# Optimization experiments

Measured on AMD Instinct MI355X. Metric: run time of the kernel, lower is better.

The kernel has to match this reference:

```python
import jax, jax.numpy as jnp
import numpy as np

B, M, N, T = 16, 16, 32, 80


def setup_inputs() -> dict:
    key = jax.random.key(0)
    ks = jax.random.split(key, 20)
    p = lambda k, shp: jax.random.normal(k, shp, jnp.float32) * 0.05
    return {
        "ego_traj": jax.random.normal(ks[0], (B, M, T, 6), jnp.float32),
        "ego_encoding": jax.random.normal(ks[1], (B, 256), jnp.float32),
        "agents_traj": jax.random.normal(ks[2], (B, M, N, T, 3), jnp.float32),
        "agents_states": jax.random.normal(ks[3], (B, N, 11), jnp.float32),
        # interaction_feature_encoder: Linear(10,64) -> ReLU -> Linear(64,256)
        "enc_w1": p(ks[4], (10, 64)), "enc_b1": p(ks[5], (64,)),
        "enc_w2": p(ks[6], (64, 256)), "enc_b2": p(ks[7], (256,)),
        # interaction_feature_decoder: Linear(256,64) -> ELU -> Linear(64,4) -> Sigmoid
        "dec_w1": p(ks[8], (256, 64)), "dec_b1": p(ks[9], (64,)),
        "dec_w2": p(ks[10], (64, 4)), "dec_b2": p(ks[11], (4,)),
        # weights_decoder: Linear(256,64) -> ELU -> Linear(64,8) -> Softplus
        "wd_w1": p(ks[12], (256, 64)), "wd_b1": p(ks[13], (64,)),
        "wd_w2": p(ks[14], (64, 8)), "wd_b2": p(ks[15], (8,)),
        "timesteps": 80,
    }


def reference(ego_traj, ego_encoding, agents_traj, agents_states,
              enc_w1, enc_b1, enc_w2, enc_b2,
              dec_w1, dec_b1, dec_w2, dec_b2,
              wd_w1, wd_b1, wd_w2, wd_b2, timesteps):
    Tm = timesteps
    # ---- hardcoded ego features: B,M,4 ----
    speed = ego_traj[:, :, :Tm, 3]
    acc = ego_traj[:, :, :Tm, 4]
    jerk = jnp.diff(acc, axis=-1) / 0.1
    jerk = jnp.concatenate([jerk[:, :, :1], jerk], axis=-1)
    curvature = ego_traj[:, :, :Tm, 5]
    lat_acc = speed ** 2 * curvature
    hard = jnp.stack([
        -jnp.clip(speed.mean(-1), 0.0, 15.0) / 15.0,
        jnp.clip(jnp.abs(acc).mean(-1), 0.0, 4.0) / 4.0,
        jnp.clip(jnp.abs(jerk).mean(-1), 0.0, 6.0) / 6.0,
        jnp.clip(jnp.abs(lat_acc).mean(-1), 0.0, 5.0) / 5.0,
    ], axis=-1)  # B,M,4

    # ---- latent interaction features (vectorized over M) ----
    agent_mask = (agents_states.sum(-1) != 0).astype(ego_traj.dtype)  # B,N
    ry = agents_traj[:, :, :, :Tm, 2] - ego_traj[:, :, None, :Tm, 2]  # B,M,N,T
    ry = jnp.arctan2(jnp.sin(ry), jnp.cos(ry))
    rp = agents_traj[:, :, :, :Tm, :2] - ego_traj[:, :, None, :Tm, :2]
    rp = jnp.stack([rp[..., 0] * jnp.cos(ry), rp[..., 1] * jnp.sin(ry)], axis=-1)
    av = jnp.diff(agents_traj[:, :, :, :Tm, :2], axis=-2) / 0.1
    av = jnp.concatenate([av[:, :, :, :1, :], av], axis=-2)
    evx = ego_traj[:, :, :Tm, 3] * jnp.cos(ego_traj[:, :, :Tm, 2])  # B,M,T
    evy = ego_traj[:, :, :Tm, 3] * jnp.sin(ego_traj[:, :, :Tm, 2])
    rv = jnp.stack([(av[..., 0] - evx[:, :, None]) * jnp.cos(ry),
                    (av[..., 1] - evy[:, :, None]) * jnp.sin(ry)], axis=-1)
    rel = jnp.concatenate([rp, ry[..., None], rv], axis=-1)  # B,M,N,T,5
    aattr = jnp.broadcast_to(agents_states[:, None, :, None, 6:], rel.shape[:4] + (5,))
    attr = jnp.concatenate([rel, aattr], axis=-1) * agent_mask[:, None, :, None, None]  # B,M,N,T,10
    h = jax.nn.relu(attr @ enc_w1 + enc_b1) @ enc_w2 + enc_b2  # B,M,N,T,256
    feat = h.max(axis=2).mean(axis=2)  # max over agents, mean over time -> B,M,256
    inter = jax.nn.sigmoid(jax.nn.elu(feat @ dec_w1 + dec_b1) @ dec_w2 + dec_b2)  # B,M,4

    # ---- weights (variable_cost=False -> ones_like encoding) ----
    enc_in = jnp.ones_like(ego_encoding)
    weights = jax.nn.softplus(jax.nn.elu(enc_in @ wd_w1 + wd_b1) @ wd_w2 + wd_b2)  # B,8

    # ---- collision cost: B,M ----
    dist = jnp.linalg.norm(ego_traj[:, :, None, :Tm, :2] - agents_traj[:, :, :, :Tm, :2], axis=-1)
    coll = (jnp.exp(-0.2 * dist ** 2) * agent_mask[:, None, :, None]).sum((-1, -2))

    feats = jnp.concatenate([hard, inter], axis=-1)  # B,M,8
    scores = -jnp.sum(feats * weights[:, None, :], axis=-1) - 10.0 * coll
    ego_mask = ego_traj.sum(-1).sum(-1) != 0  # B,M
    scores = jnp.where(ego_mask, scores, -jnp.inf)
    return scores, weights
```

## Files before the change

### kernel.cpp

```cpp
#include <hip/hip_runtime.h>
#include <hip/hip_fp16.h>
#include <math.h>
#include <string.h>

typedef __attribute__((ext_vector_type(8))) short short8;
typedef __attribute__((ext_vector_type(8))) _Float16 f16x8;
typedef __attribute__((ext_vector_type(4))) _Float16 h4;
typedef __attribute__((ext_vector_type(2))) _Float16 h2;
typedef __attribute__((ext_vector_type(4))) float f32x4;

#define NB 16
#define NM 16
#define NN 32
#define NT 80
#define TC 16
#define NP 5
#define CH 4
#define NCH 8

#define WS_WTS 0
#define WS_BF 16
#define WS_BB 8208
#define WS_BASE 24592
#define WS_BM_STRIDE 1344
#define WS_SC_OFF 1280

__device__ __forceinline__ short f2h(float f) {
  _Float16 h = (_Float16)f;
  short s; memcpy(&s, &h, 2); return s;
}
__device__ __forceinline__ unsigned h2bits(h2 h) {
  unsigned u; memcpy(&u, &h, 4); return u;
}
__device__ __forceinline__ h2 bits2h(unsigned u) {
  h2 h; memcpy(&h, &u, 4); return h;
}

__global__ void prep_kernel(const float* __restrict__ agents_states,
                            const float* __restrict__ enc_w1,
                            const float* __restrict__ enc_b1,
                            const float* __restrict__ enc_w2,
                            const float* __restrict__ wd_w1,
                            const float* __restrict__ wd_b1,
                            const float* __restrict__ wd_w2,
                            const float* __restrict__ wd_b2,
                            float* __restrict__ ws,
                            float* __restrict__ out) {
  const int blk = blockIdx.x;
  const int tid = threadIdx.x;
  if (blk < NB) {
    __shared__ float smask[NN];
    if (tid < NN) {
      const float* st = agents_states + ((size_t)blk * NN + tid) * 11;
      float s = 0.f;
      for (int i = 0; i < 11; ++i) s += st[i];
      smask[tid] = (s != 0.f) ? 1.f : 0.f;
    }
    __syncthreads();
    h2* bb = reinterpret_cast<h2*>(ws + WS_BB) + blk * (NN * 32);
    for (int e = tid; e < NN * 32; e += 256) {
      int n = e >> 5, jp = e & 31;
      const float* st = agents_states + ((size_t)blk * NN + n) * 11 + 6;
      float v[2];
#pragma unroll
      for (int hh = 0; hh < 2; ++hh) {
        int j = jp * 2 + hh;
        float acc = st[0] * enc_w1[5 * 64 + j] + st[1] * enc_w1[6 * 64 + j] +
                    st[2] * enc_w1[7 * 64 + j] + st[3] * enc_w1[8 * 64 + j] +
                    st[4] * enc_w1[9 * 64 + j];
        v[hh] = smask[n] * acc + enc_b1[j];
      }
      h2 r; r[0] = (_Float16)v[0]; r[1] = (_Float16)v[1];
      bb[e] = r;
    }
  } else if (blk < NB + 8) {
    const int g = tid >> 6;
    const int lane = tid & 63;
    const int s = (blk - NB) * 4 + g;
    const int wv = s >> 3, jb = (s >> 1) & 3, kt = s & 1;
    const int col = wv * 64 + jb * 16 + (lane & 15);
    const int krow = (lane >> 4) * 8;
    short8 v;
#pragma unroll
    for (int j = 0; j < 8; ++j)
      v[j] = f2h(enc_w2[(kt * 32 + krow + j) * 256 + col]);
    reinterpret_cast<short8*>(ws + WS_BF)[s * 64 + lane] = v;
  } else {
    __shared__ float sh[64];
    if (tid < 64) {
      float acc = wd_b1[tid];
      for (int i = 0; i < 256; ++i) acc += wd_w1[i * 64 + tid];
      sh[tid] = acc > 0.f ? acc : expm1f(acc);
    }
    __syncthreads();
    if (tid < 8) {
      float acc = wd_b2[tid];
      for (int k = 0; k < 64; ++k) acc += sh[k] * wd_w2[k * 8 + tid];
      float sp = log1pf(__expf(acc));
      ws[WS_WTS + tid] = sp;
      for (int b = 0; b < NB; ++b) out[NB * NM + b * 8 + tid] = sp;
    }
  }
}

__global__ __launch_bounds__(256, 4) void score_partial(
    const float* __restrict__ ego_traj,
    const float* __restrict__ agents_traj,
    const float* __restrict__ agents_states,
    const float* __restrict__ enc_w1,
    float* __restrict__ ws)
{
  __shared__ h4 s_r01[NN][TC];
  __shared__ h4 s_r23[NN][TC];
  __shared__ h2 s_r4[NN][TC];
  __shared__ uint2 s_bb[NN][16];
  __shared__ __align__(16) char s_hid[CH][TC * 128];
  __shared__ float s_ego[TC][5];
  __shared__ float s_acc[TC + 2];
  __shared__ float s_spd[TC], s_lat[TC], s_egos[TC];
  __shared__ float s_mask[NN];
  __shared__ float s_cw[4];

  const int p = blockIdx.x;
  const int bm = blockIdx.y;
  const int t0 = p * TC;
  const int b = bm >> 4;
  const int tid = threadIdx.x;
  const int lane = tid & 63;
  const int wv = tid >> 6;

  float* ws_bm = ws + WS_BASE + (size_t)bm * WS_BM_STRIDE;

  if (tid < TC) {
    int i = tid;
    const float* e = ego_traj + ((size_t)bm * NT + (t0 + i)) * 6;
    float ex = e[0], ey = e[1], eh = e[2], spd = e[3], acc = e[4], cur = e[5];
    s_ego[i][0] = ex; s_ego[i][1] = ey; s_ego[i][2] = eh;
    s_ego[i][3] = spd * __cosf(eh);
    s_ego[i][4] = spd * __sinf(eh);
    s_spd[i] = spd;
    s_acc[i + 1] = acc;
    s_lat[i] = fabsf(spd * spd * cur);
    s_egos[i] = ex + ey + eh + spd + acc + cur;
  } else if (tid == TC) {
    int tp = (p == 0) ? 0 : (t0 - 1);
    s_acc[0] = ego_traj[((size_t)bm * NT + tp) * 6 + 4];
  } else if (tid >= 64 && tid < 64 + NN) {
    int n = tid - 64;
    const float* st = agents_states + ((size_t)b * NN + n) * 11;
    float s = 0.f;
    for (int i = 0; i < 11; ++i) s += st[i];
    s_mask[n] = (s != 0.f) ? 1.f : 0.f;
  }
  {
    const uint2* bbt = reinterpret_cast<const uint2*>(ws + WS_BB) + b * 512;
#pragma unroll
    for (int k = 0; k < 2; ++k) {
      int e = tid + k * 256;
      s_bb[e >> 4][e & 15] = bbt[e];
    }
  }

  const int jq = tid & 15;
  const int tt = tid >> 4;
  const int j0 = jq * 4;

  f16x8 Bf[4][2];
  {
    const f16x8* bft = reinterpret_cast<const f16x8*>(ws + WS_BF);
#pragma unroll
    for (int jb = 0; jb < 4; ++jb)
#pragma unroll
      for (int kt = 0; kt < 2; ++kt)
        Bf[jb][kt] = bft[((wv * 4 + jb) * 2 + kt) * 64 + lane];
  }

  h2 w1h[5][2];
#pragma unroll
  for (int f = 0; f < 5; ++f)
#pragma unroll
    for (int jp = 0; jp < 2; ++jp) {
      h2 r;
      r[0] = (_Float16)enc_w1[f * 64 + j0 + jp * 2];
      r[1] = (_Float16)enc_w1[f * 64 + j0 + jp * 2 + 1];
      w1h[f][jp] = r;
    }
  __syncthreads();

  {
    float collacc = 0.f;
    const float* atraj = agents_traj + (size_t)bm * (NN * NT * 3);
#pragma unroll
    for (int k = 0; k < 2; ++k) {
      int pp = tid + k * 256;
      int n = pp >> 4;
      int i = pp & 15;
      int tg = t0 + i;
      const float* bp = atraj + n * (NT * 3) + tg * 3;
      float ax = bp[0], ay = bp[1], ah = bp[2];
      float avx, avy;
      if (tg == 0) { avx = (bp[3] - ax) * 10.f; avy = (bp[4] - ay) * 10.f; }
      else         { avx = (ax - bp[-3]) * 10.f; avy = (ay - bp[-2]) * 10.f; }
      float ex = s_ego[i][0], ey = s_ego[i][1], eh = s_ego[i][2];
      float evx = s_ego[i][3], evy = s_ego[i][4];
      float m = s_mask[n];
      float ryr = ah - eh;
      float w = ryr - 6.283185307179586f * rintf(ryr * 0.15915494309189535f);
      float cy = __cosf(ryr), sy = __sinf(ryr);
      float dx = ax - ex, dy = ay - ey;
      float r0 = dx * cy * m, r1 = dy * sy * m, r2 = w * m;
      float r3 = (avx - evx) * cy * m, r4 = (avy - evy) * sy * m;
      h4 v01, v23; h2 v4;
      v01[0] = v01[1] = (_Float16)r0; v01[2] = v01[3] = (_Float16)r1;
      v23[0] = v23[1] = (_Float16)r2; v23[2] = v23[3] = (_Float16)r3;
      v4[0] = v4[1] = (_Float16)r4;
      s_r01[n][i] = v01;
      s_r23[n][i] = v23;
      s_r4[n][i] = v4;
      collacc += __expf(-0.2f * (dx * dx + dy * dy)) * m;
    }
#pragma unroll
    for (int off = 1; off < 64; off <<= 1) collacc += __shfl_xor(collacc, off);
    if (lane == 0) s_cw[wv] = collacc;
  }

  if (tid >= 251) {
    int which = tid - 251;
    float s = 0.f;
    if (which == 0)      { for (int i = 0; i < TC; ++i) s += s_spd[i]; }
    else if (which == 1) { for (int i = 0; i < TC; ++i) s += fabsf(s_acc[i + 1]); }
    else if (which == 2) {
      for (int i = 0; i < TC; ++i) {
        int ia = (p == 0 && i == 0) ? 2 : (i + 1);
        s += fabsf((s_acc[ia] - s_acc[ia - 1]) * 10.f);
      }
    }
    else if (which == 3) { for (int i = 0; i < TC; ++i) s += s_lat[i]; }
    else                 { for (int i = 0; i < TC; ++i) s += s_egos[i]; }
    ws_bm[WS_SC_OFF + p * 8 + which] = s;
  }

  const int tl = lane & 15, kg = lane >> 4;
  const int swr = (tl & 7) << 4;
  const int aoff0 = tl * 128 + ((kg * 16) ^ swr);
  const int aoff1 = tl * 128 + ((64 + kg * 16) ^ swr);
  const int wbyte = tt * 128 + ((jq * 8) ^ ((tt & 7) << 4));

  h2 z2; z2[0] = z2[1] = (_Float16)0.f;

  auto compute_chunk = [&](int c) {
#pragma unroll
    for (int nn = 0; nn < CH; ++nn) {
      const int n = c * CH + nn;
      h4 r01 = s_r01[n][tt];
      h4 r23 = s_r23[n][tt];
      h2 r4 = s_r4[n][tt];
      uint2 bb = s_bb[n][jq];
      h2 a0 = __builtin_shufflevector(r01, r01, 0, 1);
      h2 a1 = __builtin_shufflevector(r01, r01, 2, 3);
      h2 a2 = __builtin_shufflevector(r23, r23, 0, 1);
      h2 a3 = __builtin_shufflevector(r23, r23, 2, 3);
      uint2 u;
#pragma unroll
      for (int jp = 0; jp < 2; ++jp) {
        h2 ha = bits2h(jp ? bb.y : bb.x);
        ha = a0 * w1h[0][jp] + ha;
        ha = a1 * w1h[1][jp] + ha;
        ha = a2 * w1h[2][jp] + ha;
        ha = a3 * w1h[3][jp] + ha;
        ha = r4 * w1h[4][jp] + ha;
        ha = __builtin_elementwise_max(ha, z2);
        if (jp == 0) u.x = h2bits(ha); else u.y = h2bits(ha);
      }
      *reinterpret_cast<uint2*>(&s_hid[nn][0] + wbyte) = u;
    }
  };

  f32x4 rmax[4];
#pragma unroll
  for (int jb = 0; jb < 4; ++jb)
    rmax[jb] = f32x4{-3e38f, -3e38f, -3e38f, -3e38f};

  auto mfma_step = [&]() {
#pragma unroll
    for (int nn = 0; nn < CH; ++nn) {
      const char* slab = &s_hid[nn][0];
      f16x8 A0 = *reinterpret_cast<const f16x8*>(slab + aoff0);
      f16x8 A1 = *reinterpret_cast<const f16x8*>(slab + aoff1);
#pragma unroll
      for (int jb = 0; jb < 4; ++jb) {
        f32x4 c = {0.f, 0.f, 0.f, 0.f};
        c = __builtin_amdgcn_mfma_f32_16x16x32_f16(A0, Bf[jb][0], c, 0, 0, 0);
        c = __builtin_amdgcn_mfma_f32_16x16x32_f16(A1, Bf[jb][1], c, 0, 0, 0);
        rmax[jb] = __builtin_elementwise_max(rmax[jb], c);
      }
    }
  };

  __syncthreads();

  for (int c = 0; c < NCH; ++c) {
    compute_chunk(c);
    __syncthreads();
    mfma_step();
    __syncthreads();
  }

  {
#pragma unroll
    for (int jb = 0; jb < 4; ++jb) {
      float s = (rmax[jb][0] + rmax[jb][1]) + (rmax[jb][2] + rmax[jb][3]);
      s += __shfl_xor(s, 16);
      s += __shfl_xor(s, 32);
      if (lane < 16)
        ws_bm[p * 256 + wv * 64 + jb * 16 + lane] = s;
    }
  }
  if (tid == 0)
    ws_bm[WS_SC_OFF + p * 8 + 5] = s_cw[0] + s_cw[1] + s_cw[2] + s_cw[3];
}

__global__ void combine_kernel(const float* __restrict__ ws,
                               const float* __restrict__ enc_b2,
                               const float* __restrict__ dec_w1,
                               const float* __restrict__ dec_b1,
                               const float* __restrict__ dec_w2,
                               const float* __restrict__ dec_b2,
                               float* __restrict__ out_scores) {
  __shared__ float s_feat[256];
  __shared__ float s_dh[64];
  __shared__ float s_hard[4];
  __shared__ float s_inter[4];
  __shared__ float s_mc[2];
  const int bm = blockIdx.x;
  const int tid = threadIdx.x;
  const float* wb = ws + WS_BASE + (size_t)bm * WS_BM_STRIDE;

  for (int c = tid; c < 256; c += 64) {
    float f = 0.f;
#pragma unroll
    for (int pp = 0; pp < NP; ++pp) f += wb[pp * 256 + c];
    s_feat[c] = f * (1.f / NT) + enc_b2[c];
  }
  const float* sc = wb + WS_SC_OFF;
  if (tid < 6) {
    float s = 0.f;
#pragma unroll
    for (int pp = 0; pp < NP; ++pp) s += sc[pp * 8 + tid];
    if (tid == 0) s_hard[0] = -fminf(fmaxf(s * (1.f / NT), 0.f), 15.f) * (1.f / 15.f);
    if (tid == 1) s_hard[1] = fminf(fmaxf(s * (1.f / NT), 0.f), 4.f) * 0.25f;
    if (tid == 2) s_hard[2] = fminf(fmaxf(s * (1.f / NT), 0.f), 6.f) * (1.f / 6.f);
    if (tid == 3) s_hard[3] = fminf(fmaxf(s * (1.f / NT), 0.f), 5.f) * 0.2f;
    if (tid == 4) s_mc[0] = s;
    if (tid == 5) s_mc[1] = s;
  }
  __syncthreads();

  {
    float a0 = 0.f, a1 = 0.f, a2 = 0.f, a3 = 0.f;
    for (int i = 0; i < 256; i += 4) {
      a0 += s_feat[i + 0] * dec_w1[(i + 0) * 64 + tid];
      a1 += s_feat[i + 1] * dec_w1[(i + 1) * 64 + tid];
      a2 += s_feat[i + 2] * dec_w1[(i + 2) * 64 + tid];
      a3 += s_feat[i + 3] * dec_w1[(i + 3) * 64 + tid];
    }
    float acc = dec_b1[tid] + ((a0 + a1) + (a2 + a3));
    s_dh[tid] = acc > 0.f ? acc : expm1f(acc);
  }
  __syncthreads();

  if (tid < 4) {
    float acc = dec_b2[tid];
    for (int k = 0; k < 64; ++k) acc += s_dh[k] * dec_w2[k * 4 + tid];
    s_inter[tid] = 1.f / (1.f + __expf(-acc));
  }
  __syncthreads();

  if (tid == 0) {
    const float* wts = ws + WS_WTS;
    float scv = 0.f;
#pragma unroll
    for (int i = 0; i < 4; ++i) scv += s_hard[i] * wts[i];
#pragma unroll
    for (int i = 0; i < 4; ++i) scv += s_inter[i] * wts[4 + i];
    scv = -scv - 10.f * s_mc[1];
    if (s_mc[0] == 0.f) scv = -INFINITY;
    out_scores[bm] = scv;
  }
}

extern "C" void kernel_launch(void* const* d_in, const int* in_sizes, int n_in,
                              void* d_out, int out_size, void* d_ws, size_t ws_size,
                              hipStream_t stream) {
  const float* ego_traj      = (const float*)d_in[0];
  const float* agents_traj   = (const float*)d_in[2];
  const float* agents_states = (const float*)d_in[3];
  const float* enc_w1 = (const float*)d_in[4];
  const float* enc_b1 = (const float*)d_in[5];
  const float* enc_w2 = (const float*)d_in[6];
  const float* enc_b2 = (const float*)d_in[7];
  const float* dec_w1 = (const float*)d_in[8];
  const float* dec_b1 = (const float*)d_in[9];
  const float* dec_w2 = (const float*)d_in[10];
  const float* dec_b2 = (const float*)d_in[11];
  const float* wd_w1 = (const float*)d_in[12];
  const float* wd_b1 = (const float*)d_in[13];
  const float* wd_w2 = (const float*)d_in[14];
  const float* wd_b2 = (const float*)d_in[15];

  float* out = (float*)d_out;
  float* ws = (float*)d_ws;

  prep_kernel<<<NB + 9, 256, 0, stream>>>(agents_states, enc_w1, enc_b1, enc_w2,
                                          wd_w1, wd_b1, wd_w2, wd_b2, ws, out);
  dim3 grid(NP, NB * NM);
  score_partial<<<grid, 256, 0, stream>>>(
      ego_traj, agents_traj, agents_states, enc_w1, ws);
  combine_kernel<<<NB * NM, 64, 0, stream>>>(
      ws, enc_b2, dec_w1, dec_b1, dec_w2, dec_b2, out);
}
```

Measured before the change: 43.37 us.

## Compute layer-1 hidden directly in MFMA A-fragment registers, dropping shared staging

Each wave now builds its own MFMA A operands for the first encoder layer in registers, reading relative features and per-agent bias from shared memory. This removes the shared s_hid staging buffer and the two block barriers per chunk of agents. In exchange every one of the four waves recomputes the same 16x64 hidden tile, quadrupling the packed-FP16 FMA work. Register pressure also rises, so launch bounds drop from 4 to 2 blocks per SIMD.

```diff
diff --git a/kernel.cpp b/kernel.cpp
--- a/kernel.cpp
+++ b/kernel.cpp
@@ -5,7 +5,6 @@
 
 typedef __attribute__((ext_vector_type(8))) short short8;
 typedef __attribute__((ext_vector_type(8))) _Float16 f16x8;
-typedef __attribute__((ext_vector_type(4))) _Float16 h4;
 typedef __attribute__((ext_vector_type(2))) _Float16 h2;
 typedef __attribute__((ext_vector_type(4))) float f32x4;
 
@@ -15,8 +14,6 @@
 #define NT 80
 #define TC 16
 #define NP 5
-#define CH 4
-#define NCH 8
 
 #define WS_WTS 0
 #define WS_BF 16
@@ -28,12 +25,6 @@
 __device__ __forceinline__ short f2h(float f) {
   _Float16 h = (_Float16)f;
   short s; memcpy(&s, &h, 2); return s;
-}
-__device__ __forceinline__ unsigned h2bits(h2 h) {
-  unsigned u; memcpy(&u, &h, 4); return u;
-}
-__device__ __forceinline__ h2 bits2h(unsigned u) {
-  h2 h; memcpy(&h, &u, 4); return h;
 }
 
 __global__ void prep_kernel(const float* __restrict__ agents_states,
@@ -103,18 +94,16 @@
   }
 }
 
-__global__ __launch_bounds__(256, 4) void score_partial(
+__global__ __launch_bounds__(256, 2) void score_partial(
     const float* __restrict__ ego_traj,
     const float* __restrict__ agents_traj,
     const float* __restrict__ agents_states,
     const float* __restrict__ enc_w1,
     float* __restrict__ ws)
 {
-  __shared__ h4 s_r01[NN][TC];
-  __shared__ h4 s_r23[NN][TC];
-  __shared__ h2 s_r4[NN][TC];
-  __shared__ uint2 s_bb[NN][16];
-  __shared__ __align__(16) char s_hid[CH][TC * 128];
+  __shared__ __align__(16) _Float16 s_rel8[NN][TC][8];
+  __shared__ h2 s_rel2[NN][TC];
+  __shared__ __align__(16) char s_bb[NN][128];
   __shared__ float s_ego[TC][5];
   __shared__ float s_acc[TC + 2];
   __shared__ float s_spd[TC], s_lat[TC], s_egos[TC];
@@ -154,16 +143,16 @@
   }
   {
     const uint2* bbt = reinterpret_cast<const uint2*>(ws + WS_BB) + b * 512;
+    uint2* dst = reinterpret_cast<uint2*>(&s_bb[0][0]);
 #pragma unroll
     for (int k = 0; k < 2; ++k) {
       int e = tid + k * 256;
-      s_bb[e >> 4][e & 15] = bbt[e];
-    }
-  }
-
-  const int jq = tid & 15;
-  const int tt = tid >> 4;
-  const int j0 = jq * 4;
+      dst[e] = bbt[e];
+    }
+  }
+
+  const int tl = lane & 15;
+  const int kg = lane >> 4;
 
   f16x8 Bf[4][2];
   {
@@ -175,15 +164,17 @@
         Bf[jb][kt] = bft[((wv * 4 + jb) * 2 + kt) * 64 + lane];
   }
 
-  h2 w1h[5][2];
+  h2 w1A[5][4], w1B[5][4];
 #pragma unroll
   for (int f = 0; f < 5; ++f)
 #pragma unroll
-    for (int jp = 0; jp < 2; ++jp) {
-      h2 r;
-      r[0] = (_Float16)enc_w1[f * 64 + j0 + jp * 2];
-      r[1] = (_Float16)enc_w1[f * 64 + j0 + jp * 2 + 1];
-      w1h[f][jp] = r;
+    for (int q = 0; q < 4; ++q) {
+      h2 ra, rb;
+      ra[0] = (_Float16)enc_w1[f * 64 + 8 * kg + 2 * q];
+      ra[1] = (_Float16)enc_w1[f * 64 + 8 * kg + 2 * q + 1];
+      rb[0] = (_Float16)enc_w1[f * 64 + 32 + 8 * kg + 2 * q];
+      rb[1] = (_Float16)enc_w1[f * 64 + 32 + 8 * kg + 2 * q + 1];
+      w1A[f][q] = ra; w1B[f][q] = rb;
     }
   __syncthreads();
 
@@ -208,15 +199,17 @@
       float w = ryr - 6.283185307179586f * rintf(ryr * 0.15915494309189535f);
       float cy = __cosf(ryr), sy = __sinf(ryr);
       float dx = ax - ex, dy = ay - ey;
-      float r0 = dx * cy * m, r1 = dy * sy * m, r2 = w * m;
-      float r3 = (avx - evx) * cy * m, r4 = (avy - evy) * sy * m;
-      h4 v01, v23; h2 v4;
-      v01[0] = v01[1] = (_Float16)r0; v01[2] = v01[3] = (_Float16)r1;
-      v23[0] = v23[1] = (_Float16)r2; v23[2] = v23[3] = (_Float16)r3;
-      v4[0] = v4[1] = (_Float16)r4;
-      s_r01[n][i] = v01;
-      s_r23[n][i] = v23;
-      s_r4[n][i] = v4;
+      _Float16 r0 = (_Float16)(dx * cy * m);
+      _Float16 r1 = (_Float16)(dy * sy * m);
+      _Float16 r2 = (_Float16)(w * m);
+      _Float16 r3 = (_Float16)((avx - evx) * cy * m);
+      _Float16 r4 = (_Float16)((avy - evy) * sy * m);
+      f16x8 v8;
+      v8[0] = r0; v8[1] = r0; v8[2] = r1; v8[3] = r1;
+      v8[4] = r2; v8[5] = r2; v8[6] = r3; v8[7] = r3;
+      *reinterpret_cast<f16x8*>(&s_rel8[n][i][0]) = v8;
+      h2 v4; v4[0] = r4; v4[1] = r4;
+      s_rel2[n][i] = v4;
       collacc += __expf(-0.2f * (dx * dx + dy * dy)) * m;
     }
 #pragma unroll
@@ -240,70 +233,51 @@
     ws_bm[WS_SC_OFF + p * 8 + which] = s;
   }
 
-  const int tl = lane & 15, kg = lane >> 4;
-  const int swr = (tl & 7) << 4;
-  const int aoff0 = tl * 128 + ((kg * 16) ^ swr);
-  const int aoff1 = tl * 128 + ((64 + kg * 16) ^ swr);
-  const int wbyte = tt * 128 + ((jq * 8) ^ ((tt & 7) << 4));
+  __syncthreads();
 
   h2 z2; z2[0] = z2[1] = (_Float16)0.f;
-
-  auto compute_chunk = [&](int c) {
-#pragma unroll
-    for (int nn = 0; nn < CH; ++nn) {
-      const int n = c * CH + nn;
-      h4 r01 = s_r01[n][tt];
-      h4 r23 = s_r23[n][tt];
-      h2 r4 = s_r4[n][tt];
-      uint2 bb = s_bb[n][jq];
-      h2 a0 = __builtin_shufflevector(r01, r01, 0, 1);
-      h2 a1 = __builtin_shufflevector(r01, r01, 2, 3);
-      h2 a2 = __builtin_shufflevector(r23, r23, 0, 1);
-      h2 a3 = __builtin_shufflevector(r23, r23, 2, 3);
-      uint2 u;
-#pragma unroll
-      for (int jp = 0; jp < 2; ++jp) {
-        h2 ha = bits2h(jp ? bb.y : bb.x);
-        ha = a0 * w1h[0][jp] + ha;
-        ha = a1 * w1h[1][jp] + ha;
-        ha = a2 * w1h[2][jp] + ha;
-        ha = a3 * w1h[3][jp] + ha;
-        ha = r4 * w1h[4][jp] + ha;
-        ha = __builtin_elementwise_max(ha, z2);
-        if (jp == 0) u.x = h2bits(ha); else u.y = h2bits(ha);
-      }
-      *reinterpret_cast<uint2*>(&s_hid[nn][0] + wbyte) = u;
-    }
-  };
-
   f32x4 rmax[4];
 #pragma unroll
   for (int jb = 0; jb < 4; ++jb)
     rmax[jb] = f32x4{-3e38f, -3e38f, -3e38f, -3e38f};
 
-  auto mfma_step = [&]() {
-#pragma unroll
-    for (int nn = 0; nn < CH; ++nn) {
-      const char* slab = &s_hid[nn][0];
-      f16x8 A0 = *reinterpret_cast<const f16x8*>(slab + aoff0);
-      f16x8 A1 = *reinterpret_cast<const f16x8*>(slab + aoff1);
-#pragma unroll
-      for (int jb = 0; jb < 4; ++jb) {
-        f32x4 c = {0.f, 0.f, 0.f, 0.f};
-        c = __builtin_amdgcn_mfma_f32_16x16x32_f16(A0, Bf[jb][0], c, 0, 0, 0);
-        c = __builtin_amdgcn_mfma_f32_16x16x32_f16(A1, Bf[jb][1], c, 0, 0, 0);
-        rmax[jb] = __builtin_elementwise_max(rmax[jb], c);
-      }
-    }
-  };
-
-  __syncthreads();
-
-  for (int c = 0; c < NCH; ++c) {
-    compute_chunk(c);
-    __syncthreads();
-    mfma_step();
-    __syncthreads();
+#pragma unroll 4
+  for (int n = 0; n < NN; ++n) {
+    f16x8 r8 = *reinterpret_cast<const f16x8*>(&s_rel8[n][tl][0]);
+    h2 r4v = s_rel2[n][tl];
+    f16x8 bb0 = *reinterpret_cast<const f16x8*>(&s_bb[n][kg * 16]);
+    f16x8 bb1 = *reinterpret_cast<const f16x8*>(&s_bb[n][64 + kg * 16]);
+    h2 f0 = __builtin_shufflevector(r8, r8, 0, 1);
+    h2 f1 = __builtin_shufflevector(r8, r8, 2, 3);
+    h2 f2 = __builtin_shufflevector(r8, r8, 4, 5);
+    h2 f3 = __builtin_shufflevector(r8, r8, 6, 7);
+    f16x8 A0, A1;
+#pragma unroll
+    for (int q = 0; q < 4; ++q) {
+      h2 a; a[0] = bb0[2 * q]; a[1] = bb0[2 * q + 1];
+      a = f0 * w1A[0][q] + a;
+      a = f1 * w1A[1][q] + a;
+      a = f2 * w1A[2][q] + a;
+      a = f3 * w1A[3][q] + a;
+      a = r4v * w1A[4][q] + a;
+      a = __builtin_elementwise_max(a, z2);
+      A0[2 * q] = a[0]; A0[2 * q + 1] = a[1];
+      h2 c; c[0] = bb1[2 * q]; c[1] = bb1[2 * q + 1];
+      c = f0 * w1B[0][q] + c;
+      c = f1 * w1B[1][q] + c;
+      c = f2 * w1B[2][q] + c;
+      c = f3 * w1B[3][q] + c;
+      c = r4v * w1B[4][q] + c;
+      c = __builtin_elementwise_max(c, z2);
+      A1[2 * q] = c[0]; A1[2 * q + 1] = c[1];
+    }
+#pragma unroll
+    for (int jb = 0; jb < 4; ++jb) {
+      f32x4 cacc = {0.f, 0.f, 0.f, 0.f};
+      cacc = __builtin_amdgcn_mfma_f32_16x16x32_f16(A0, Bf[jb][0], cacc, 0, 0, 0);
+      cacc = __builtin_amdgcn_mfma_f32_16x16x32_f16(A1, Bf[jb][1], cacc, 0, 0, 0);
+      rmax[jb] = __builtin_elementwise_max(rmax[jb], cacc);
+    }
   }
 
   {
```

Measured after the change: 57.50 us. +32.6%, slower.
